# Kernel tuning notes

Measured on AMD Instinct MI355X. Metric: run time of the kernel, lower is better.

The kernel has to match this reference:

```python
import jax, jax.numpy as jnp
import numpy as np

G = 512  # number of graphs per batch


def gcn_conv(x, edge_index, edge_attr, W):
    # x:[N,Fin], edge_index:[2,E], edge_attr:[E,1], W:[Fin,Fout]
    n = x.shape[0]
    loop = jnp.arange(n)
    row = jnp.concatenate([edge_index[0], loop])
    col = jnp.concatenate([edge_index[1], loop])
    w = jnp.concatenate([edge_attr[:, 0], jnp.ones((n,), x.dtype)])
    deg = jnp.zeros((n,), x.dtype).at[col].add(jnp.ones_like(w))
    dinv = jnp.clip(deg, 1e-12) ** -0.5
    norm = dinv[row] * w * dinv[col]
    h = x @ W  # [N,Fout]
    msg = h[row] * norm[:, None]  # [E+N,Fout] gather+scale
    return jnp.zeros_like(h).at[col].add(msg)  # scatter-add


def mean_pool(x, batch):
    s = jnp.zeros((G, x.shape[1]), x.dtype).at[batch].add(x)
    c = jnp.zeros((G,), x.dtype).at[batch].add(1.0)
    return s / jnp.clip(c, 1.0)[:, None]


def setup_inputs() -> dict:
    key = jax.random.key(0)
    ks = jax.random.split(key, 32)
    Nd, Ed, Np, Ep = 100000, 500000, 200000, 2000000
    d = {
        "drug_x": jax.random.normal(ks[0], (Nd, 78), jnp.float32),
        "drug_edge_index": jax.random.randint(ks[1], (2, Ed), 0, Nd),
        "drug_edge_attr": jax.random.uniform(ks[2], (Ed, 1), jnp.float32),
        "drug_batch": jnp.sort(jax.random.randint(ks[3], (Nd,), 0, G)),
        "protein_x": jax.random.normal(ks[4], (Np, 20), jnp.float32),
        "protein_edge_index": jax.random.randint(ks[5], (2, Ep), 0, Np),
        "protein_edge_attr": jax.random.uniform(ks[6], (Ep, 1), jnp.float32),
        "protein_batch": jnp.sort(jax.random.randint(ks[7], (Np,), 0, G)),
    }
    def w(k, i, o):
        return jax.random.normal(k, (i, o), jnp.float32) / np.sqrt(i)
    d.update({
        "dW1": w(ks[8], 78, 78), "dW2": w(ks[9], 78, 156), "dW3": w(ks[10], 156, 312),
        "dL1_w": w(ks[11], 312, 1024), "dL1_b": jnp.zeros((1024,), jnp.float32),
        "dL2_w": w(ks[12], 1024, 64), "dL2_b": jnp.zeros((64,), jnp.float32),
        "pW1": w(ks[13], 20, 20), "pW2": w(ks[14], 20, 40), "pW3": w(ks[15], 40, 80),
        "pL1_w": w(ks[16], 80, 1024), "pL1_b": jnp.zeros((1024,), jnp.float32),
        "pL2_w": w(ks[17], 1024, 64), "pL2_b": jnp.zeros((64,), jnp.float32),
        "fW1": w(ks[18], 128, 1024), "fb1": jnp.zeros((1024,), jnp.float32),
        "fW2": w(ks[19], 1024, 512), "fb2": jnp.zeros((512,), jnp.float32),
        "fW3": w(ks[20], 512, 1), "fb3": jnp.zeros((1,), jnp.float32),
    })
    return d


def reference(drug_x, drug_edge_index, drug_edge_attr, drug_batch,
              protein_x, protein_edge_index, protein_edge_attr, protein_batch,
              dW1, dW2, dW3, dL1_w, dL1_b, dL2_w, dL2_b,
              pW1, pW2, pW3, pL1_w, pL1_b, pL2_w, pL2_b,
              fW1, fb1, fW2, fb2, fW3, fb3):
    relu = jax.nn.relu
    x = relu(gcn_conv(drug_x, drug_edge_index, drug_edge_attr, dW1))
    x = relu(gcn_conv(x, drug_edge_index, drug_edge_attr, dW2))
    x = relu(gcn_conv(x, drug_edge_index, drug_edge_attr, dW3))
    x = mean_pool(x, drug_batch)
    x = relu(x @ dL1_w + dL1_b)
    x = relu(x @ dL2_w + dL2_b)
    p = relu(gcn_conv(protein_x, protein_edge_index, protein_edge_attr, pW1))
    p = relu(gcn_conv(p, protein_edge_index, protein_edge_attr, pW2))
    p = relu(gcn_conv(p, protein_edge_index, protein_edge_attr, pW3))
    p = mean_pool(p, protein_batch)
    p = relu(p @ pL1_w + pL1_b)
    p = relu(p @ pL2_w + pL2_b)
    c = jnp.concatenate([x, p], axis=1)  # [G,128]
    h = relu(c @ fW1 + fb1)
    h = relu(h @ fW2 + fb2)
    out = h @ fW3 + fb3  # [G,1]
    return out[:, 0]
```

## Files before the change

kernel.cpp:

```cpp
#include <hip/hip_runtime.h>
#include <math.h>

#define NGRAPH 512

typedef __attribute__((ext_vector_type(8))) __bf16 bf16x8;
typedef __attribute__((ext_vector_type(4))) float f32x4;

__device__ __forceinline__ unsigned short f2bf(float x) {
    unsigned int u = __float_as_uint(x);
    u = (u + 0x7fffu + ((u >> 16) & 1u)) >> 16;
    return (unsigned short)u;
}
__device__ __forceinline__ float bf2f(unsigned short b) {
    return __uint_as_float(((unsigned int)b) << 16);
}

static inline unsigned grid_for(size_t n, int block = 256) {
    return (unsigned)((n + block - 1) / block);
}

__global__ void fill_i32(int* __restrict__ p, int v, size_t n) {
    size_t i = blockIdx.x * (size_t)blockDim.x + threadIdx.x;
    if (i < n) p[i] = v;
}

__global__ void hist_kernel(const int* __restrict__ col, int E, int* __restrict__ cnt) {
    size_t i = blockIdx.x * (size_t)blockDim.x + threadIdx.x;
    if (i < (size_t)E) atomicAdd(&cnt[col[i]], 1);
}

__global__ void wcvt_t(const float* __restrict__ in, unsigned short* __restrict__ out,
                       int K, int N, int KPAD) {
    int i = blockIdx.x * blockDim.x + threadIdx.x;
    if (i >= N * KPAD) return;
    int n = i / KPAD, k = i - n * KPAD;
    out[i] = (k < K) ? f2bf(in[(size_t)k * N + n]) : (unsigned short)0;
}

__global__ void scan_pass1(const int* __restrict__ in, int* __restrict__ bsum,
                           float* __restrict__ dinv, int n) {
    __shared__ int sdata[256];
    int tid = threadIdx.x;
    int i = blockIdx.x * 256 + tid;
    int v = (i < n) ? in[i] : 0;
    if (i < n) dinv[i] = 1.0f / sqrtf((float)v + 1.0f);
    sdata[tid] = v;
    __syncthreads();
    for (int s = 128; s > 0; s >>= 1) {
        if (tid < s) sdata[tid] += sdata[tid + s];
        __syncthreads();
    }
    if (tid == 0) bsum[blockIdx.x] = sdata[0];
}

__global__ void scan_pass2(int* __restrict__ bsum, int nb) {
    __shared__ int s[1024];
    int tid = threadIdx.x;
    int v = (tid < nb) ? bsum[tid] : 0;
    s[tid] = v;
    __syncthreads();
    for (int ofs = 1; ofs < 1024; ofs <<= 1) {
        int t = (tid >= ofs) ? s[tid - ofs] : 0;
        __syncthreads();
        s[tid] += t;
        __syncthreads();
    }
    if (tid < nb) bsum[tid] = s[tid] - v;
}

__global__ void scan_pass3(int* __restrict__ pos, const int* __restrict__ bsum, int n) {
    __shared__ int sdata[256];
    int tid = threadIdx.x;
    int i = blockIdx.x * 256 + tid;
    int v = (i < n) ? pos[i] : 0;
    sdata[tid] = v;
    __syncthreads();
    for (int ofs = 1; ofs < 256; ofs <<= 1) {
        int t = (tid >= ofs) ? sdata[tid - ofs] : 0;
        __syncthreads();
        sdata[tid] += t;
        __syncthreads();
    }
    if (i < n) pos[i] = sdata[tid] - v + bsum[blockIdx.x];
}

__global__ void csr_fill(const int* __restrict__ row, const int* __restrict__ col,
                         const float* __restrict__ attr, const float* __restrict__ dinv,
                         int* __restrict__ pos, int2* __restrict__ rcp, int E) {
    size_t i = blockIdx.x * (size_t)blockDim.x + threadIdx.x;
    if (i >= (size_t)E) return;
    int r = row[i], c = col[i];
    int slot = atomicAdd(&pos[c], 1);
    rcp[slot] = make_int2(r, __float_as_int(dinv[r] * attr[i] * dinv[c]));
}

template <int V, int LPG, int F, int LDI, int LDO, bool INBF>
__global__ void gather_bf(const int* __restrict__ pos, const int2* __restrict__ rcp,
                          const void* __restrict__ Xv, const float* __restrict__ dinv,
                          unsigned short* __restrict__ AGG, int N) {
    constexpr int gpb = 256 / LPG;
    int grp = threadIdx.x / LPG;
    if (grp >= gpb) return;
    int gid = blockIdx.x * gpb + grp;
    int lane = threadIdx.x - grp * LPG;
    if (gid >= N) return;

    auto load_row = [&](int r, float* dst) {
        if (INBF) {
            const unsigned short* X = (const unsigned short*)Xv;
            if (V == 2) {
                unsigned int u = *reinterpret_cast<const unsigned int*>(X + (size_t)r * LDI + lane * 2);
                dst[0] = bf2f((unsigned short)(u & 0xffffu));
                dst[1] = bf2f((unsigned short)(u >> 16));
            } else {
                uint2 u = *reinterpret_cast<const uint2*>(X + (size_t)r * LDI + lane * 4);
                dst[0] = bf2f((unsigned short)(u.x & 0xffffu));
                dst[1] = bf2f((unsigned short)(u.x >> 16));
                dst[2] = bf2f((unsigned short)(u.y & 0xffffu));
                dst[3] = bf2f((unsigned short)(u.y >> 16));
            }
        } else {
            const float* X = (const float*)Xv;
            if (V == 2) {
                float2 u = *reinterpret_cast<const float2*>(X + (size_t)r * LDI + lane * 2);
                dst[0] = u.x; dst[1] = u.y;
            } else {
                float4 u = *reinterpret_cast<const float4*>(X + (size_t)r * LDI + lane * 4);
                dst[0] = u.x; dst[1] = u.y; dst[2] = u.z; dst[3] = u.w;
            }
        }
    };

    int start = (gid == 0) ? 0 : pos[gid - 1];
    int end = pos[gid];
    float s = dinv[gid];
    float s2 = s * s;
    float acc[V];
    load_row(gid, acc);
#pragma unroll
    for (int j = 0; j < V; ++j) acc[j] *= s2;
    int t = start;
    for (; t + 4 <= end; t += 4) {
        int2 e0 = rcp[t], e1 = rcp[t + 1], e2 = rcp[t + 2], e3 = rcp[t + 3];
        float c0 = __int_as_float(e0.y), c1 = __int_as_float(e1.y);
        float c2 = __int_as_float(e2.y), c3 = __int_as_float(e3.y);
        float h0[V], h1[V], h2[V], h3[V];
        load_row(e0.x, h0); load_row(e1.x, h1); load_row(e2.x, h2); load_row(e3.x, h3);
#pragma unroll
        for (int j = 0; j < V; ++j) {
            float v = fmaf(c0, h0[j], acc[j]);
            v = fmaf(c1, h1[j], v);
            v = fmaf(c2, h2[j], v);
            acc[j] = fmaf(c3, h3[j], v);
        }
    }
    for (; t < end; ++t) {
        int2 e = rcp[t];
        float cf = __int_as_float(e.y);
        float h[V];
        load_row(e.x, h);
#pragma unroll
        for (int j = 0; j < V; ++j) acc[j] = fmaf(cf, h[j], acc[j]);
    }
    unsigned short* op = AGG + (size_t)gid * LDO + lane * V;
    if (V == 2) {
        unsigned int p = (unsigned int)f2bf(acc[0]) | ((unsigned int)f2bf(acc[1]) << 16);
        *reinterpret_cast<unsigned int*>(op) = p;
    } else {
        uint2 p;
        p.x = (unsigned int)f2bf(acc[0]) | ((unsigned int)f2bf(acc[1]) << 16);
        p.y = (unsigned int)f2bf(acc[2]) | ((unsigned int)f2bf(acc[3]) << 16);
        *reinterpret_cast<uint2*>(op) = p;
    }
    constexpr int PAD = LDO - F;
#pragma unroll
    for (int p = lane; p < PAD; p += LPG) AGG[(size_t)gid * LDO + F + p] = 0;
}

template <int KPAD, int BN>
__global__ __launch_bounds__(256) void tgemm_mfma(
        const unsigned short* __restrict__ A, const unsigned short* __restrict__ Wt,
        unsigned short* __restrict__ C, int M, int N, int ldc) {
    constexpr int CH = KPAD / 8;
    constexpr int KSTEPS = KPAD / 32;
    constexpr int NI = (BN / 2) / 16;
    __shared__ unsigned short As[128 * KPAD];
    const int tid = threadIdx.x;
    const int m0 = blockIdx.y * 128;
    const int n0 = blockIdx.x * BN;

    for (int idx = tid; idx < 128 * CH; idx += 256) {
        int m = idx / CH;
        int c = idx - m * CH;
        int gm = m0 + m;
        uint4 v = make_uint4(0u, 0u, 0u, 0u);
        if (gm < M) v = *reinterpret_cast<const uint4*>(A + (size_t)gm * KPAD + c * 8);
        int cs = c ^ (m & 7);
        *reinterpret_cast<uint4*>(&As[m * KPAD + cs * 8]) = v;
    }
    __syncthreads();

    const int wid = tid >> 6;
    const int l = tid & 63;
    const int wm = wid >> 1, wn = wid & 1;
    const int lr = l & 15, lg = l >> 4;

    f32x4 acc[4][NI];
#pragma unroll
    for (int i = 0; i < 4; ++i)
#pragma unroll
        for (int j = 0; j < NI; ++j) acc[i][j] = (f32x4){0.f, 0.f, 0.f, 0.f};

    for (int ks = 0; ks < KSTEPS; ++ks) {
        bf16x8 a[4], b[NI];
#pragma unroll
        for (int mi = 0; mi < 4; ++mi) {
            int row = wm * 64 + mi * 16 + lr;
            int cs = (ks * 4 + lg) ^ (row & 7);
            a[mi] = *reinterpret_cast<const bf16x8*>(&As[row * KPAD + cs * 8]);
        }
#pragma unroll
        for (int ni = 0; ni < NI; ++ni) {
            int gn = n0 + wn * (BN / 2) + ni * 16 + lr;
            int gns = (gn < N) ? gn : (N - 1);
            b[ni] = *reinterpret_cast<const bf16x8*>(
                &Wt[(size_t)gns * KPAD + ks * 32 + lg * 8]);
        }
#pragma unroll
        for (int mi = 0; mi < 4; ++mi)
#pragma unroll
            for (int ni = 0; ni < NI; ++ni)
                acc[mi][ni] = __builtin_amdgcn_mfma_f32_16x16x32_bf16(
                    a[mi], b[ni], acc[mi][ni], 0, 0, 0);
    }

#pragma unroll
    for (int mi = 0; mi < 4; ++mi) {
#pragma unroll
        for (int ni = 0; ni < NI; ++ni) {
#pragma unroll
            for (int j = 0; j < 4; ++j) {
                int gm = m0 + wm * 64 + mi * 16 + lg * 4 + j;
                int gn = n0 + wn * (BN / 2) + ni * 16 + lr;
                if (gm < M && gn < N)
                    C[(size_t)gm * ldc + gn] = f2bf(fmaxf(acc[mi][ni][j], 0.0f));
            }
        }
    }
}

__global__ void pool_mean_bf(const unsigned short* __restrict__ X, const int* __restrict__ batch,
                             float* __restrict__ out, int N, int F) {
    int g = blockIdx.x;
    int lo = 0, hi = N;
    while (lo < hi) { int mid = (lo + hi) >> 1; if (batch[mid] < g) lo = mid + 1; else hi = mid; }
    int s0 = lo;
    hi = N;
    while (lo < hi) { int mid = (lo + hi) >> 1; if (batch[mid] < g + 1) lo = mid + 1; else hi = mid; }
    int s1 = lo;
    int c = s1 - s0;
    float inv = 1.0f / (float)(c > 0 ? c : 1);
    for (int f = threadIdx.x; f < F; f += blockDim.x) {
        float acc = 0.0f;
        for (int n = s0; n < s1; ++n) acc += fmaxf(bf2f(X[(size_t)n * F + f]), 0.0f);
        out[(size_t)g * F + f] = acc * inv;
    }
}

template <int K, int NOUT>
__global__ __launch_bounds__(64 * (K / 4)) void fused_conv(
        const int* __restrict__ pos, const int2* __restrict__ rcp,
        const float* __restrict__ X, const float* __restrict__ dinv,
        const float* __restrict__ W, float* __restrict__ Y, int N) {
    constexpr int LPG = K / 4;
    constexpr int NTHREADS = 64 * LPG;
    union U { float4 v; float a[4]; };
    __shared__ float Ws[K][NOUT];
    __shared__ float Ag[64][K + 4];
    const int tid = threadIdx.x;
    const int nid0 = blockIdx.x * 64;

    for (int i = tid; i < K * NOUT; i += NTHREADS) Ws[i / NOUT][i % NOUT] = W[i];

    int grp = tid / LPG, lane = tid % LPG;
    int gid = nid0 + grp;
    if (gid < N) {
        int start = (gid == 0) ? 0 : pos[gid - 1];
        int end = pos[gid];
        float s = dinv[gid];
        float s2 = s * s;
        U acc;
        acc.v = *reinterpret_cast<const float4*>(X + (size_t)gid * K + lane * 4);
#pragma unroll
        for (int j = 0; j < 4; ++j) acc.a[j] *= s2;
        int t = start;
        for (; t + 4 <= end; t += 4) {
            int2 e0 = rcp[t], e1 = rcp[t + 1], e2 = rcp[t + 2], e3 = rcp[t + 3];
            float c0 = __int_as_float(e0.y), c1 = __int_as_float(e1.y);
            float c2 = __int_as_float(e2.y), c3 = __int_as_float(e3.y);
            U h0, h1, h2, h3;
            h0.v = *reinterpret_cast<const float4*>(X + (size_t)e0.x * K + lane * 4);
            h1.v = *reinterpret_cast<const float4*>(X + (size_t)e1.x * K + lane * 4);
            h2.v = *reinterpret_cast<const float4*>(X + (size_t)e2.x * K + lane * 4);
            h3.v = *reinterpret_cast<const float4*>(X + (size_t)e3.x * K + lane * 4);
#pragma unroll
            for (int j = 0; j < 4; ++j) {
                float v = fmaf(c0, h0.a[j], acc.a[j]);
                v = fmaf(c1, h1.a[j], v);
                v = fmaf(c2, h2.a[j], v);
                acc.a[j] = fmaf(c3, h3.a[j], v);
            }
        }
        for (; t < end; ++t) {
            int2 e = rcp[t];
            float cf = __int_as_float(e.y);
            U h;
            h.v = *reinterpret_cast<const float4*>(X + (size_t)e.x * K + lane * 4);
#pragma unroll
            for (int j = 0; j < 4; ++j) acc.a[j] = fmaf(cf, h.a[j], acc.a[j]);
        }
        *reinterpret_cast<float4*>(&Ag[grp][lane * 4]) = acc.v;
    }
    __syncthreads();

    for (int idx = tid; idx < 64 * NOUT; idx += NTHREADS) {
        int nl = idx / NOUT, n = idx % NOUT;
        int g = nid0 + nl;
        if (g < N) {
            float acc = 0.0f;
#pragma unroll
            for (int k = 0; k < K; ++k) acc = fmaf(Ag[nl][k], Ws[k][n], acc);
            Y[(size_t)g * NOUT + n] = fmaxf(acc, 0.0f);
        }
    }
}

__global__ void pool_mean_s(const float* __restrict__ X, const int* __restrict__ batch,
                            float* __restrict__ out, int N, int F, int S) {
    __shared__ float red[256];
    int g = blockIdx.x;
    int lo = 0, hi = N;
    while (lo < hi) { int mid = (lo + hi) >> 1; if (batch[mid] < g) lo = mid + 1; else hi = mid; }
    int s0 = lo;
    hi = N;
    while (lo < hi) { int mid = (lo + hi) >> 1; if (batch[mid] < g + 1) lo = mid + 1; else hi = mid; }
    int s1 = lo;
    int c = s1 - s0;
    float inv = 1.0f / (float)(c > 0 ? c : 1);
    int t = threadIdx.x;
    int stripe = t / F;
    int f = t - stripe * F;
    float acc = 0.0f;
    if (stripe < S) {
        for (int n = s0 + stripe; n < s1; n += S)
            acc += fmaxf(X[(size_t)n * F + f], 0.0f);
    }
    red[t] = acc;
    __syncthreads();
    if (t < F) {
        float v = red[t];
        for (int s = 1; s < S; ++s) v += red[t + s * F];
        out[(size_t)g * F + t] = v * inv;
    }
}

template <bool RELU_OUT>
__global__ __launch_bounds__(256) void skinny_gemm4(
        const float* __restrict__ A, const float* __restrict__ W,
        const float* __restrict__ bias, float* __restrict__ C,
        int K, int M, int ldc, int coff) {
    __shared__ float As[4][1024];
    __shared__ float red[4][64][4];
    const int tid = threadIdx.x;
    const int m_l = tid & 63;
    const int q = tid >> 6;
    const int g0 = blockIdx.y * 4;
    const int m0 = blockIdx.x * 64;

    for (int idx = tid; idx < 4 * K; idx += 256)
        As[idx / K][idx % K] = A[(size_t)(g0 + idx / K) * K + idx % K];
    __syncthreads();

    const int Kq = (K + 3) >> 2;
    const int ks = q * Kq;
    const int ke = (ks + Kq < K) ? ks + Kq : K;
    const int m = m0 + m_l;
    float acc[4] = {0.0f, 0.0f, 0.0f, 0.0f};
    if (m < M) {
        for (int k = ks; k < ke; ++k) {
            float w = W[(size_t)k * M + m];
            acc[0] = fmaf(As[0][k], w, acc[0]);
            acc[1] = fmaf(As[1][k], w, acc[1]);
            acc[2] = fmaf(As[2][k], w, acc[2]);
            acc[3] = fmaf(As[3][k], w, acc[3]);
        }
    }
#pragma unroll
    for (int g = 0; g < 4; ++g) red[q][m_l][g] = acc[g];
    __syncthreads();
    if (q == 0 && m < M) {
        float b = bias[m];
#pragma unroll
        for (int g = 0; g < 4; ++g) {
            float v = red[0][m_l][g] + red[1][m_l][g] + red[2][m_l][g] + red[3][m_l][g] + b;
            if (RELU_OUT) v = fmaxf(v, 0.0f);
            C[(size_t)(g0 + g) * ldc + coff + m] = v;
        }
    }
}

__global__ void final_kernel(const float* __restrict__ A, const float* __restrict__ w,
                             const float* __restrict__ b, float* __restrict__ out, int K) {
    int wave = (blockIdx.x * blockDim.x + threadIdx.x) >> 6;
    int lane = threadIdx.x & 63;
    if (wave >= NGRAPH) return;
    const float* ar = A + (size_t)wave * K;
    float acc = 0.0f;
    for (int k = lane; k < K; k += 64) acc = fmaf(ar[k], w[k], acc);
#pragma unroll
    for (int s = 32; s > 0; s >>= 1) acc += __shfl_down(acc, s, 64);
    if (lane == 0) out[wave] = acc + b[0];
}

static void build_csr(const int* row, const int* col, const float* attr,
                      int N, int E, float* dinv, int* pos,
                      int2* rcp, int* bsum, hipStream_t stream) {
    const int B = 256;
    int nb = (N + 255) / 256;
    fill_i32<<<grid_for(N), B, 0, stream>>>(pos, 0, (size_t)N);
    hist_kernel<<<grid_for(E), B, 0, stream>>>(col, E, pos);
    scan_pass1<<<nb, B, 0, stream>>>(pos, bsum, dinv, N);
    scan_pass2<<<1, 1024, 0, stream>>>(bsum, nb);
    scan_pass3<<<nb, B, 0, stream>>>(pos, bsum, N);
    csr_fill<<<grid_for(E), B, 0, stream>>>(row, col, attr, dinv, pos, rcp, E);
}

extern "C" void kernel_launch(void* const* d_in, const int* in_sizes, int n_in,
                              void* d_out, int out_size, void* d_ws, size_t ws_size,
                              hipStream_t stream) {
    const float* drug_x  = (const float*)d_in[0];
    const int*   d_ei    = (const int*)d_in[1];
    const float* d_ea    = (const float*)d_in[2];
    const int*   d_batch = (const int*)d_in[3];
    const float* prot_x  = (const float*)d_in[4];
    const int*   p_ei    = (const int*)d_in[5];
    const float* p_ea    = (const float*)d_in[6];
    const int*   p_batch = (const int*)d_in[7];
    const float* dW1 = (const float*)d_in[8];
    const float* dW2 = (const float*)d_in[9];
    const float* dW3 = (const float*)d_in[10];
    const float* dL1_w = (const float*)d_in[11];
    const float* dL1_b = (const float*)d_in[12];
    const float* dL2_w = (const float*)d_in[13];
    const float* dL2_b = (const float*)d_in[14];
    const float* pW1 = (const float*)d_in[15];
    const float* pW2 = (const float*)d_in[16];
    const float* pW3 = (const float*)d_in[17];
    const float* pL1_w = (const float*)d_in[18];
    const float* pL1_b = (const float*)d_in[19];
    const float* pL2_w = (const float*)d_in[20];
    const float* pL2_b = (const float*)d_in[21];
    const float* fW1 = (const float*)d_in[22];
    const float* fb1 = (const float*)d_in[23];
    const float* fW2 = (const float*)d_in[24];
    const float* fb2 = (const float*)d_in[25];
    const float* fW3 = (const float*)d_in[26];
    const float* fb3 = (const float*)d_in[27];
    float* out = (float*)d_out;

    const int Nd = in_sizes[0] / 78;
    const int Ed = in_sizes[1] / 2;
    const int Np = in_sizes[4] / 20;
    const int Ep = in_sizes[5] / 2;
    const int* d_row = d_ei;
    const int* d_col = d_ei + Ed;
    const int* p_row = p_ei;
    const int* p_col = p_ei + Ep;

    float* ws = (float*)d_ws;
    size_t off = 0;
    auto align256 = [](size_t n) -> size_t { return (n + 255) & ~(size_t)255; };
    auto take = [&](size_t n) -> float* {
        float* p = ws + off;
        off += align256(n);
        return p;
    };
    float* B1      = take((size_t)Nd * 312);
    float* B2      = take((size_t)Nd * 312);
    float* dinv_d  = take((size_t)Nd);
    float* dinv_p  = take((size_t)Np);
    float* pool    = take((size_t)NGRAPH * 312);
    float* t1      = take((size_t)NGRAPH * 1024);
    float* Cbuf    = take((size_t)NGRAPH * 128);
    float* f2buf   = take((size_t)NGRAPH * 512);
    int*   bsum    = (int*)take(1056);
    int*   pos_d   = (int*)take((size_t)Nd);
    int2*  rcp_d   = (int2*)take((size_t)Ed * 2);
    unsigned short* Wt1 = (unsigned short*)take((78 * 128) / 2);
    unsigned short* Wt2 = (unsigned short*)take((156 * 128) / 2);
    unsigned short* Wt3 = (unsigned short*)take((312 * 192) / 2);
    size_t tail = align256((size_t)Np * 80);
    int*   pos_p   = (int*)(B1 + tail);
    int2*  rcp_p   = (int2*)(B1 + tail + align256((size_t)Np));
    (void)ws_size;

    unsigned short* B1u = (unsigned short*)B1;
    unsigned short* B2u = (unsigned short*)B2;

    const int B = 256;
    auto gblocks = [](int n, int gpb) -> unsigned { return (unsigned)((n + gpb - 1) / gpb); };
    auto mgrid = [](int M, int N, int BN) -> dim3 {
        return dim3((unsigned)((N + BN - 1) / BN), (unsigned)((M + 127) / 128));
    };

    build_csr(d_row, d_col, d_ea, Nd, Ed, dinv_d, pos_d, rcp_d, bsum, stream);
    wcvt_t<<<grid_for(78 * 128), B, 0, stream>>>(dW1, Wt1, 78, 78, 128);
    wcvt_t<<<grid_for(156 * 128), B, 0, stream>>>(dW2, Wt2, 78, 156, 128);
    wcvt_t<<<grid_for(312 * 192), B, 0, stream>>>(dW3, Wt3, 156, 312, 192);

    gather_bf<2, 39, 78, 78, 128, false><<<gblocks(Nd, 256 / 39), B, 0, stream>>>(
        pos_d, rcp_d, drug_x, dinv_d, B2u, Nd);
    tgemm_mfma<128, 64><<<mgrid(Nd, 78, 64), B, 0, stream>>>(B2u, Wt1, B1u, Nd, 78, 80);

    gather_bf<2, 39, 78, 80, 128, true><<<gblocks(Nd, 256 / 39), B, 0, stream>>>(
        pos_d, rcp_d, B1u, dinv_d, B2u, Nd);
    tgemm_mfma<128, 64><<<mgrid(Nd, 156, 64), B, 0, stream>>>(B2u, Wt2, B1u, Nd, 156, 156);

    gather_bf<4, 39, 156, 156, 192, true><<<gblocks(Nd, 256 / 39), B, 0, stream>>>(
        pos_d, rcp_d, B1u, dinv_d, B2u, Nd);
    tgemm_mfma<192, 64><<<mgrid(Nd, 312, 64), B, 0, stream>>>(B2u, Wt3, B1u, Nd, 312, 312);

    pool_mean_bf<<<NGRAPH, B, 0, stream>>>(B1u, d_batch, pool, Nd, 312);

    skinny_gemm4<true><<<dim3(16, NGRAPH / 4), B, 0, stream>>>(pool, dL1_w, dL1_b, t1, 312, 1024, 1024, 0);
    skinny_gemm4<true><<<dim3(1, NGRAPH / 4), B, 0, stream>>>(t1, dL2_w, dL2_b, Cbuf, 1024, 64, 128, 0);

    build_csr(p_row, p_col, p_ea, Np, Ep, dinv_p, pos_p, rcp_p, bsum, stream);

    fused_conv<20, 20><<<gblocks(Np, 64), 320, 0, stream>>>(
        pos_p, rcp_p, prot_x, dinv_p, pW1, B1, Np);
    fused_conv<20, 40><<<gblocks(Np, 64), 320, 0, stream>>>(
        pos_p, rcp_p, B1, dinv_p, pW2, B2, Np);
    fused_conv<40, 80><<<gblocks(Np, 64), 640, 0, stream>>>(
        pos_p, rcp_p, B2, dinv_p, pW3, B1, Np);

    pool_mean_s<<<NGRAPH, B, 0, stream>>>(B1, p_batch, pool, Np, 80, 3);

    skinny_gemm4<true><<<dim3(16, NGRAPH / 4), B, 0, stream>>>(pool, pL1_w, pL1_b, t1, 80, 1024, 1024, 0);
    skinny_gemm4<true><<<dim3(1, NGRAPH / 4), B, 0, stream>>>(t1, pL2_w, pL2_b, Cbuf, 1024, 64, 128, 64);

    skinny_gemm4<true><<<dim3(16, NGRAPH / 4), B, 0, stream>>>(Cbuf, fW1, fb1, t1, 128, 1024, 1024, 0);
    skinny_gemm4<true><<<dim3(8, NGRAPH / 4), B, 0, stream>>>(t1, fW2, fb2, f2buf, 1024, 512, 512, 0);
    final_kernel<<<grid_for((size_t)NGRAPH * 64), B, 0, stream>>>(f2buf, fW3, fb3, out, 512);
}
```

Measured before the change: 1.111 ms.

## Store protein conv activations in bf16 and split mean pooling across blocks

```diff
diff --git a/kernel.cpp b/kernel.cpp
--- a/kernel.cpp
+++ b/kernel.cpp
@@ -20,6 +20,11 @@
 }
 
 __global__ void fill_i32(int* __restrict__ p, int v, size_t n) {
+    size_t i = blockIdx.x * (size_t)blockDim.x + threadIdx.x;
+    if (i < n) p[i] = v;
+}
+
+__global__ void fill_f32(float* __restrict__ p, float v, size_t n) {
     size_t i = blockIdx.x * (size_t)blockDim.x + threadIdx.x;
     if (i < n) p[i] = v;
 }
@@ -249,34 +254,56 @@
     }
 }
 
-__global__ void pool_mean_bf(const unsigned short* __restrict__ X, const int* __restrict__ batch,
-                             float* __restrict__ out, int N, int F) {
+template <int F2, int SUB>
+__global__ void pool_part_bf(const unsigned short* __restrict__ X, const int* __restrict__ batch,
+                             float* __restrict__ pool, int N, int PB) {
+    int g = blockIdx.x / PB;
+    int st = blockIdx.x - g * PB;
+    int tid = threadIdx.x;
+    int p = tid % F2;
+    int sub = tid / F2;
+    if (sub >= SUB) return;
+    int lo = 0, hi = N;
+    while (lo < hi) { int mid = (lo + hi) >> 1; if (batch[mid] < g) lo = mid + 1; else hi = mid; }
+    int s0 = lo;
+    hi = N;
+    while (lo < hi) { int mid = (lo + hi) >> 1; if (batch[mid] < g + 1) lo = mid + 1; else hi = mid; }
+    int s1 = lo;
+    const int F = 2 * F2;
+    int stride = PB * SUB;
+    float a0 = 0.0f, a1 = 0.0f;
+    for (int n = s0 + st * SUB + sub; n < s1; n += stride) {
+        unsigned int u = *reinterpret_cast<const unsigned int*>(X + (size_t)n * F + 2 * p);
+        a0 += fmaxf(bf2f((unsigned short)(u & 0xffffu)), 0.0f);
+        a1 += fmaxf(bf2f((unsigned short)(u >> 16)), 0.0f);
+    }
+    atomicAdd(&pool[(size_t)g * F + 2 * p], a0);
+    atomicAdd(&pool[(size_t)g * F + 2 * p + 1], a1);
+}
+
+__global__ void pool_div_g(float* __restrict__ pool, const int* __restrict__ batch,
+                           int N, int F) {
     int g = blockIdx.x;
     int lo = 0, hi = N;
     while (lo < hi) { int mid = (lo + hi) >> 1; if (batch[mid] < g) lo = mid + 1; else hi = mid; }
     int s0 = lo;
     hi = N;
     while (lo < hi) { int mid = (lo + hi) >> 1; if (batch[mid] < g + 1) lo = mid + 1; else hi = mid; }
-    int s1 = lo;
-    int c = s1 - s0;
+    int c = lo - s0;
     float inv = 1.0f / (float)(c > 0 ? c : 1);
-    for (int f = threadIdx.x; f < F; f += blockDim.x) {
-        float acc = 0.0f;
-        for (int n = s0; n < s1; ++n) acc += fmaxf(bf2f(X[(size_t)n * F + f]), 0.0f);
-        out[(size_t)g * F + f] = acc * inv;
-    }
-}
-
-template <int K, int NOUT>
-__global__ __launch_bounds__(64 * (K / 4)) void fused_conv(
+    for (int f = threadIdx.x; f < F; f += blockDim.x)
+        pool[(size_t)g * F + f] *= inv;
+}
+
+template <int K, int NOUT, bool INBF>
+__global__ __launch_bounds__(64 * (K / 4)) void fused_conv_bf(
         const int* __restrict__ pos, const int2* __restrict__ rcp,
-        const float* __restrict__ X, const float* __restrict__ dinv,
-        const float* __restrict__ W, float* __restrict__ Y, int N) {
+        const void* __restrict__ Xv, const float* __restrict__ dinv,
+        const float* __restrict__ W, unsigned short* __restrict__ Y, int N) {
     constexpr int LPG = K / 4;
     constexpr int NTHREADS = 64 * LPG;
-    union U { float4 v; float a[4]; };
     __shared__ float Ws[K][NOUT];
-    __shared__ float Ag[64][K + 4];
+    __shared__ float Ag[64][K + 8];
     const int tid = threadIdx.x;
     const int nid0 = blockIdx.x * 64;
 
@@ -284,42 +311,56 @@
 
     int grp = tid / LPG, lane = tid % LPG;
     int gid = nid0 + grp;
+
+    auto load_row = [&](int r, float* dst) {
+        if (INBF) {
+            const unsigned short* X = (const unsigned short*)Xv;
+            uint2 u = *reinterpret_cast<const uint2*>(X + (size_t)r * K + lane * 4);
+            dst[0] = bf2f((unsigned short)(u.x & 0xffffu));
+            dst[1] = bf2f((unsigned short)(u.x >> 16));
+            dst[2] = bf2f((unsigned short)(u.y & 0xffffu));
+            dst[3] = bf2f((unsigned short)(u.y >> 16));
+        } else {
+            const float* X = (const float*)Xv;
+            float4 u = *reinterpret_cast<const float4*>(X + (size_t)r * K + lane * 4);
+            dst[0] = u.x; dst[1] = u.y; dst[2] = u.z; dst[3] = u.w;
+        }
+    };
+
     if (gid < N) {
         int start = (gid == 0) ? 0 : pos[gid - 1];
         int end = pos[gid];
         float s = dinv[gid];
         float s2 = s * s;
-        U acc;
-        acc.v = *reinterpret_cast<const float4*>(X + (size_t)gid * K + lane * 4);
-#pragma unroll
-        for (int j = 0; j < 4; ++j) acc.a[j] *= s2;
+        float acc[4];
+        load_row(gid, acc);
+#pragma unroll
+        for (int j = 0; j < 4; ++j) acc[j] *= s2;
         int t = start;
         for (; t + 4 <= end; t += 4) {
             int2 e0 = rcp[t], e1 = rcp[t + 1], e2 = rcp[t + 2], e3 = rcp[t + 3];
             float c0 = __int_as_float(e0.y), c1 = __int_as_float(e1.y);
             float c2 = __int_as_float(e2.y), c3 = __int_as_float(e3.y);
-            U h0, h1, h2, h3;
-            h0.v = *reinterpret_cast<const float4*>(X + (size_t)e0.x * K + lane * 4);
-            h1.v = *reinterpret_cast<const float4*>(X + (size_t)e1.x * K + lane * 4);
-            h2.v = *reinterpret_cast<const float4*>(X + (size_t)e2.x * K + lane * 4);
-            h3.v = *reinterpret_cast<const float4*>(X + (size_t)e3.x * K + lane * 4);
+            float h0[4], h1[4], h2[4], h3[4];
+            load_row(e0.x, h0); load_row(e1.x, h1); load_row(e2.x, h2); load_row(e3.x, h3);
 #pragma unroll
             for (int j = 0; j < 4; ++j) {
-                float v = fmaf(c0, h0.a[j], acc.a[j]);
-                v = fmaf(c1, h1.a[j], v);
-                v = fmaf(c2, h2.a[j], v);
-                acc.a[j] = fmaf(c3, h3.a[j], v);
+                float v = fmaf(c0, h0[j], acc[j]);
+                v = fmaf(c1, h1[j], v);
+                v = fmaf(c2, h2[j], v);
+                acc[j] = fmaf(c3, h3[j], v);
             }
         }
         for (; t < end; ++t) {
             int2 e = rcp[t];
             float cf = __int_as_float(e.y);
-            U h;
-            h.v = *reinterpret_cast<const float4*>(X + (size_t)e.x * K + lane * 4);
-#pragma unroll
-            for (int j = 0; j < 4; ++j) acc.a[j] = fmaf(cf, h.a[j], acc.a[j]);
-        }
-        *reinterpret_cast<float4*>(&Ag[grp][lane * 4]) = acc.v;
+            float h[4];
+            load_row(e.x, h);
+#pragma unroll
+            for (int j = 0; j < 4; ++j) acc[j] = fmaf(cf, h[j], acc[j]);
+        }
+#pragma unroll
+        for (int j = 0; j < 4; ++j) Ag[grp][lane * 4 + j] = acc[j];
     }
     __syncthreads();
 
@@ -330,37 +371,8 @@
             float acc = 0.0f;
 #pragma unroll
             for (int k = 0; k < K; ++k) acc = fmaf(Ag[nl][k], Ws[k][n], acc);
-            Y[(size_t)g * NOUT + n] = fmaxf(acc, 0.0f);
-        }
-    }
-}
-
-__global__ void pool_mean_s(const float* __restrict__ X, const int* __restrict__ batch,
-                            float* __restrict__ out, int N, int F, int S) {
-    __shared__ float red[256];
-    int g = blockIdx.x;
-    int lo = 0, hi = N;
-    while (lo < hi) { int mid = (lo + hi) >> 1; if (batch[mid] < g) lo = mid + 1; else hi = mid; }
-    int s0 = lo;
-    hi = N;
-    while (lo < hi) { int mid = (lo + hi) >> 1; if (batch[mid] < g + 1) lo = mid + 1; else hi = mid; }
-    int s1 = lo;
-    int c = s1 - s0;
-    float inv = 1.0f / (float)(c > 0 ? c : 1);
-    int t = threadIdx.x;
-    int stripe = t / F;
-    int f = t - stripe * F;
-    float acc = 0.0f;
-    if (stripe < S) {
-        for (int n = s0 + stripe; n < s1; n += S)
-            acc += fmaxf(X[(size_t)n * F + f], 0.0f);
-    }
-    red[t] = acc;
-    __syncthreads();
-    if (t < F) {
-        float v = red[t];
-        for (int s = 1; s < S; ++s) v += red[t + s * F];
-        out[(size_t)g * F + t] = v * inv;
+            Y[(size_t)g * NOUT + n] = f2bf(fmaxf(acc, 0.0f));
+        }
     }
 }
 
@@ -530,21 +542,25 @@
         pos_d, rcp_d, B1u, dinv_d, B2u, Nd);
     tgemm_mfma<192, 64><<<mgrid(Nd, 312, 64), B, 0, stream>>>(B2u, Wt3, B1u, Nd, 312, 312);
 
-    pool_mean_bf<<<NGRAPH, B, 0, stream>>>(B1u, d_batch, pool, Nd, 312);
+    fill_f32<<<grid_for((size_t)NGRAPH * 312), B, 0, stream>>>(pool, 0.0f, (size_t)NGRAPH * 312);
+    pool_part_bf<156, 1><<<NGRAPH * 8, B, 0, stream>>>(B1u, d_batch, pool, Nd, 8);
+    pool_div_g<<<NGRAPH, B, 0, stream>>>(pool, d_batch, Nd, 312);
 
     skinny_gemm4<true><<<dim3(16, NGRAPH / 4), B, 0, stream>>>(pool, dL1_w, dL1_b, t1, 312, 1024, 1024, 0);
     skinny_gemm4<true><<<dim3(1, NGRAPH / 4), B, 0, stream>>>(t1, dL2_w, dL2_b, Cbuf, 1024, 64, 128, 0);
 
     build_csr(p_row, p_col, p_ea, Np, Ep, dinv_p, pos_p, rcp_p, bsum, stream);
 
-    fused_conv<20, 20><<<gblocks(Np, 64), 320, 0, stream>>>(
-        pos_p, rcp_p, prot_x, dinv_p, pW1, B1, Np);
-    fused_conv<20, 40><<<gblocks(Np, 64), 320, 0, stream>>>(
-        pos_p, rcp_p, B1, dinv_p, pW2, B2, Np);
-    fused_conv<40, 80><<<gblocks(Np, 64), 640, 0, stream>>>(
-        pos_p, rcp_p, B2, dinv_p, pW3, B1, Np);
-
-    pool_mean_s<<<NGRAPH, B, 0, stream>>>(B1, p_batch, pool, Np, 80, 3);
+    fused_conv_bf<20, 20, false><<<gblocks(Np, 64), 320, 0, stream>>>(
+        pos_p, rcp_p, prot_x, dinv_p, pW1, B1u, Np);
+    fused_conv_bf<20, 40, true><<<gblocks(Np, 64), 320, 0, stream>>>(
+        pos_p, rcp_p, B1u, dinv_p, pW2, B2u, Np);
+    fused_conv_bf<40, 80, true><<<gblocks(Np, 64), 640, 0, stream>>>(
+        pos_p, rcp_p, B2u, dinv_p, pW3, B1u, Np);
+
+    fill_f32<<<grid_for((size_t)NGRAPH * 80), B, 0, stream>>>(pool, 0.0f, (size_t)NGRAPH * 80);
+    pool_part_bf<40, 6><<<NGRAPH * 8, B, 0, stream>>>(B1u, p_batch, pool, Np, 8);
+    pool_div_g<<<NGRAPH, B, 0, stream>>>(pool, p_batch, Np, 80);
 
     skinny_gemm4<true><<<dim3(16, NGRAPH / 4), B, 0, stream>>>(pool, pL1_w, pL1_b, t1, 80, 1024, 1024, 0);
     skinny_gemm4<true><<<dim3(1, NGRAPH / 4), B, 0, stream>>>(t1, pL2_w, pL2_b, Cbuf, 1024, 64, 128, 64);
```

New measurement: 1.024 ms, median of 2. 1.08x faster.
